# Optimization experiments

Measured on AMD Instinct MI355X. Metric: run time of the kernel, lower is better.

Reference implementation:

```python
import jax, jax.numpy as jnp
import numpy as np

B, N, C = 4, 2048, 1024
H = 16
HD = C // H
SCALE = HD ** -0.5


def setup_inputs() -> dict:
    key = jax.random.key(0)
    k1, k2, k3 = jax.random.split(key, 3)
    x = jax.random.normal(k1, (B, N, C), dtype=jnp.float32)
    qkv_w = jax.random.normal(k2, (3 * C, C), dtype=jnp.float32) * (C ** -0.5)
    proj_w = jax.random.normal(k3, (C, C), dtype=jnp.float32) * (C ** -0.5)
    proj_b = jnp.zeros((C,), dtype=jnp.float32)
    return {"x": x, "qkv_w": qkv_w, "proj_w": proj_w, "proj_b": proj_b}


def reference(x, qkv_w, proj_w, proj_b):
    b, n, c = x.shape
    # qkv: [B, N, 3C] -> [3, B, H, N, HD]
    qkv = jnp.einsum('bnc,dc->bnd', x, qkv_w)
    qkv = qkv.reshape(b, n, 3, H, c // H).transpose(2, 0, 3, 1, 4)
    q, k, v = qkv[0] * SCALE, qkv[1], qkv[2]
    # attention scores [B, H, N, N]
    attn = jnp.einsum('bhqd,bhkd->bhqk', q, k)
    attn = jax.nn.softmax(attn, axis=-1)
    out = jnp.einsum('bhqk,bhkd->bhqd', attn, v)  # [B, H, N, HD]
    out = out.transpose(0, 2, 1, 3).reshape(b, n, c)
    out = jnp.einsum('bnc,dc->bnd', out, proj_w) + proj_b
    return out
```

## Files before the change

kernel.cpp:

```cpp
#include <hip/hip_runtime.h>
#include <math.h>

#define B_  4
#define N_  2048
#define C_  1024
#define H_  16
#define HD_ 64
#define C3_ (3 * C_)
#define QSCALE_ 0.18033688011112042f

typedef float f32x4  __attribute__((ext_vector_type(4)));
typedef float f32x16 __attribute__((ext_vector_type(16)));
typedef short short8 __attribute__((ext_vector_type(8)));
typedef unsigned short ushort8 __attribute__((ext_vector_type(8)));
typedef unsigned int uint2v __attribute__((ext_vector_type(2)));

__device__ inline unsigned short f2bf(float f) {
    union { float f; unsigned u; } v; v.f = f;
    unsigned r = v.u + 0x7fffu + ((v.u >> 16) & 1u);
    return (unsigned short)(r >> 16);
}

__device__ inline unsigned cvtpk_bf16(float lo, float hi) {
    unsigned r;
    asm("v_cvt_pk_bf16_f32 %0, %1, %2" : "=v"(r) : "v"(lo), "v"(hi));
    return r;
}

#define GLD16(gptr, lptr) \
    __builtin_amdgcn_global_load_lds((const __attribute__((address_space(1))) unsigned int*)(gptr), \
                                     (__attribute__((address_space(3))) unsigned int*)(lptr), 16, 0, 0)

__global__ __launch_bounds__(256) void cast_bf16_k(const float* __restrict__ in,
                                                   unsigned short* __restrict__ out,
                                                   int n8, int scale_n8, float scale) {
    int i = blockIdx.x * 256 + threadIdx.x;
    if (i >= n8) return;
    float sc = (i < scale_n8) ? scale : 1.0f;
    const float4* p = (const float4*)in + (size_t)i * 2;
    float4 a = p[0], b = p[1];
    ushort8 o;
    o[0]=f2bf(a.x*sc); o[1]=f2bf(a.y*sc); o[2]=f2bf(a.z*sc); o[3]=f2bf(a.w*sc);
    o[4]=f2bf(b.x*sc); o[5]=f2bf(b.y*sc); o[6]=f2bf(b.z*sc); o[7]=f2bf(b.w*sc);
    *((ushort8*)out + i) = o;
}

__device__ inline void gemm128_core(const unsigned short* __restrict__ A,
                                    const unsigned short* __restrict__ Bm,
                                    int m0, int n0, int K,
                                    char* smem,
                                    f32x4 acc[4][4])
{
    const int tid = threadIdx.x;
    const int lane = tid & 63, w = tid >> 6;
    const int lg = lane >> 4, lr = lane & 15;
    const int wr = (w >> 1) * 64, wc = (w & 1) * 64;
    const int srow = tid >> 2;
    const int scs = (tid & 3) ^ ((srow >> 1) & 3);
    const int lgx = lg ^ ((lr >> 1) & 3);
    const unsigned wbase = (unsigned)(tid & 192) * 16;

    const unsigned short* pa0 = &A[(size_t)(m0 + srow) * K + scs * 8];
    const unsigned short* pa1 = &A[(size_t)(m0 + srow + 64) * K + scs * 8];
    const unsigned short* pb0 = &Bm[(size_t)(n0 + srow) * K + scs * 8];
    const unsigned short* pb1 = &Bm[(size_t)(n0 + srow + 64) * K + scs * 8];

    GLD16(pa0, smem + wbase);
    GLD16(pa1, smem + 4096 + wbase);
    GLD16(pb0, smem + 16384 + wbase);
    GLD16(pb1, smem + 16384 + 4096 + wbase);

    const int NT = K / 32;
    for (int t = 0; t < NT; ++t) {
        __syncthreads();
        const unsigned cur = (unsigned)(t & 1) * 8192;
        if (t + 1 < NT) {
            const unsigned nxt = 8192 - cur;
            const int ko = (t + 1) * 32;
            GLD16(pa0 + ko, smem + nxt + wbase);
            GLD16(pa1 + ko, smem + nxt + 4096 + wbase);
            GLD16(pb0 + ko, smem + 16384 + nxt + wbase);
            GLD16(pb1 + ko, smem + 16384 + nxt + 4096 + wbase);
        }
        const unsigned short* cA = (const unsigned short*)(smem + cur);
        const unsigned short* cB = (const unsigned short*)(smem + 16384 + cur);
        short8 af[4], bf[4];
#pragma unroll
        for (int i = 0; i < 4; ++i) {
            af[i] = *(const short8*)&cA[(wr + i*16 + lr) * 32 + lgx * 8];
            bf[i] = *(const short8*)&cB[(wc + i*16 + lr) * 32 + lgx * 8];
        }
#pragma unroll
        for (int i = 0; i < 4; ++i)
#pragma unroll
            for (int j = 0; j < 4; ++j)
                acc[i][j] = __builtin_amdgcn_mfma_f32_16x16x32_bf16(af[i], bf[j], acc[i][j], 0, 0, 0);
    }
}

__global__ __launch_bounds__(256) void qkv_gemm_k(const unsigned short* __restrict__ x,
                                                  const unsigned short* __restrict__ w,
                                                  unsigned short* __restrict__ outp) {
    __shared__ __align__(16) char smem[32768];
    f32x4 acc[4][4];
    f32x4 z = {0.f, 0.f, 0.f, 0.f};
#pragma unroll
    for (int i = 0; i < 4; ++i)
#pragma unroll
        for (int j = 0; j < 4; ++j) acc[i][j] = z;

    const int m0 = blockIdx.x * 128, n0 = blockIdx.y * 128;
    gemm128_core(x, w, m0, n0, C_, smem, acc);

    const int tid = threadIdx.x, lane = tid & 63, w4 = tid >> 6;
    const int lg = lane >> 4, lr = lane & 15;
    const int wc = (w4 & 1) * 64;
    const int myhalf = w4 >> 1;
    unsigned short* ep = (unsigned short*)smem;

    for (int half = 0; half < 2; ++half) {
        __syncthreads();
        if (myhalf == half) {
#pragma unroll
            for (int mi = 0; mi < 4; ++mi)
#pragma unroll
                for (int ni = 0; ni < 4; ++ni) {
                    const int col = wc + ni * 16 + lr;
                    const int r0 = mi * 16 + lg * 4;
                    unsigned p01 = cvtpk_bf16(acc[mi][ni][0], acc[mi][ni][1]);
                    unsigned p23 = cvtpk_bf16(acc[mi][ni][2], acc[mi][ni][3]);
                    ep[(r0 + 0) * 136 + col] = (unsigned short)p01;
                    ep[(r0 + 1) * 136 + col] = (unsigned short)(p01 >> 16);
                    ep[(r0 + 2) * 136 + col] = (unsigned short)p23;
                    ep[(r0 + 3) * 136 + col] = (unsigned short)(p23 >> 16);
                }
        }
        __syncthreads();
#pragma unroll
        for (int it = 0; it < 4; ++it) {
            int id = it * 256 + tid;
            int rl = id >> 4, ch = id & 15;
            ushort8 o = *(const ushort8*)&ep[rl * 136 + ch * 8];
            *(ushort8*)&outp[(size_t)(m0 + half * 64 + rl) * C3_ + n0 + ch * 8] = o;
        }
    }
}

__global__ __launch_bounds__(256) void vtrans_k(const unsigned short* __restrict__ qkvp,
                                                unsigned short* __restrict__ vt) {
    __shared__ unsigned short st[64 * 72];
    const int tid = threadIdx.x;
    const int n0 = blockIdx.x * 64;
    const int bh = blockIdx.y;
    const int bb = bh >> 4, hh = bh & 15;
    const unsigned short* V = qkvp + (size_t)bb * N_ * C3_ + 2 * C_ + hh * HD_;
    unsigned short* VT = vt + (size_t)bh * HD_ * N_;
    const int r = tid >> 2, c = tid & 3;
    ushort8 v0 = *(const ushort8*)&V[(size_t)(n0 + r) * C3_ + c * 8];
    ushort8 v1 = *(const ushort8*)&V[(size_t)(n0 + r) * C3_ + (c + 4) * 8];
    *(ushort8*)&st[r * 72 + c * 8] = v0;
    *(ushort8*)&st[r * 72 + (c + 4) * 8] = v1;
    __syncthreads();
#pragma unroll
    for (int cc = 0; cc < 2; ++cc) {
        int ch = c + cc * 4;
        ushort8 o;
#pragma unroll
        for (int j = 0; j < 8; ++j) o[j] = st[(ch * 8 + j) * 72 + r];
        *(ushort8*)&VT[(size_t)r * N_ + n0 + ch * 8] = o;
    }
}

__global__ __launch_bounds__(256) void attn_k(const unsigned short* __restrict__ qkvp,
                                              const unsigned short* __restrict__ vt,
                                              unsigned short* __restrict__ aout) {
    __shared__ __align__(16) char smem[32768];

    const int tid = threadIdx.x, lane = tid & 63, w = tid >> 6;
    const int q31 = lane & 31, hi = lane >> 5;
    const int qt = blockIdx.x, h = blockIdx.y, b = blockIdx.z;

    const unsigned short* Qrow = qkvp + (size_t)(b * N_ + qt * 128 + w * 32 + q31) * C3_ + h * HD_;
    const unsigned short* Kbase = qkvp + (size_t)(b * N_) * C3_ + C_ + h * HD_;
    const unsigned short* VT = vt + ((size_t)b * H_ + h) * ((size_t)HD_ * N_);

    short8 qf[4];
#pragma unroll
    for (int ks = 0; ks < 4; ++ks)
        qf[ks] = *(const short8*)&Qrow[ks * 16 + hi * 8];

    f32x16 O0, O1;
#pragma unroll
    for (int r = 0; r < 16; ++r) { O0[r] = 0.f; O1[r] = 0.f; }
    float l_lane = 0.f;

    const int srow = tid >> 3;
    const int scs = (tid & 7) ^ (srow & 7) ^ ((srow >> 3) & 3);
    const unsigned wbase = (unsigned)(tid & 192) * 16;

    const unsigned short* Ksrc = Kbase + (size_t)srow * C3_ + scs * 8;
    const unsigned short* Vsrc = VT + (size_t)srow * N_ + scs * 8;

    const int xq = (q31 & 7) ^ ((q31 >> 3) & 3);
    int fo[4];
#pragma unroll
    for (int ks = 0; ks < 4; ++ks)
        fo[ks] = q31 * 128 + (((2 * ks + hi) ^ xq) * 16);

    GLD16(Ksrc,                          smem + wbase);
    GLD16(Ksrc + (size_t)32 * C3_,       smem + 4096 + wbase);
    GLD16(Vsrc,                          smem + 8192 + wbase);
    GLD16(Vsrc + (size_t)32 * N_,        smem + 12288 + wbase);

    const int NT = N_ / 64;
    for (int t = 0; t < NT; ++t) {
        __syncthreads();
        const unsigned cur = (unsigned)(t & 1) * 16384;
        if (t + 1 < NT) {
            const unsigned nxt = 16384 - cur;
            const size_t k1 = (size_t)(t + 1) * 64;
            GLD16(Ksrc + k1 * C3_,              smem + nxt + wbase);
            GLD16(Ksrc + (k1 + 32) * C3_,       smem + nxt + 4096 + wbase);
            GLD16(Vsrc + k1,                    smem + nxt + 8192 + wbase);
            GLD16(Vsrc + k1 + (size_t)32 * N_,  smem + nxt + 12288 + wbase);
        }
        const char* sK = smem + cur;
        const char* sV = smem + cur + 8192;

        f32x16 S0, S1;
#pragma unroll
        for (int r = 0; r < 16; ++r) { S0[r] = 0.f; S1[r] = 0.f; }
        __builtin_amdgcn_s_setprio(1);
#pragma unroll
        for (int ks = 0; ks < 4; ++ks) {
            short8 kfa = *(const short8*)(sK + fo[ks]);
            short8 kfb = *(const short8*)(sK + 4096 + fo[ks]);
            S0 = __builtin_amdgcn_mfma_f32_32x32x16_bf16(kfa, qf[ks], S0, 0, 0, 0);
            S1 = __builtin_amdgcn_mfma_f32_32x32x16_bf16(kfb, qf[ks], S1, 0, 0, 0);
        }
        __builtin_amdgcn_s_setprio(0);

        float rs = 0.f;
#pragma unroll
        for (int r = 0; r < 16; ++r) {
            float p0 = __builtin_amdgcn_exp2f(S0[r]);
            float p1 = __builtin_amdgcn_exp2f(S1[r]);
            S0[r] = p0; S1[r] = p1;
            rs += p0 + p1;
        }
        l_lane += rs;

        short8 pB[4];
#pragma unroll
        for (int ksk = 0; ksk < 4; ++ksk) {
            const int off = (ksk & 1) * 8;
            float e0, e1, e2, e3, e4, e5, e6, e7;
            if (ksk < 2) { e0=S0[off+0]; e1=S0[off+1]; e2=S0[off+2]; e3=S0[off+3];
                           e4=S0[off+4]; e5=S0[off+5]; e6=S0[off+6]; e7=S0[off+7]; }
            else         { e0=S1[off+0]; e1=S1[off+1]; e2=S1[off+2]; e3=S1[off+3];
                           e4=S1[off+4]; e5=S1[off+5]; e6=S1[off+6]; e7=S1[off+7]; }
            unsigned a_ = cvtpk_bf16(e0, e1);
            unsigned b_ = cvtpk_bf16(e4, e5);
            unsigned c_ = cvtpk_bf16(e2, e3);
            unsigned d_ = cvtpk_bf16(e6, e7);
            uint2v r1 = __builtin_amdgcn_permlane32_swap(a_, b_, false, false);
            uint2v r2 = __builtin_amdgcn_permlane32_swap(c_, d_, false, false);
            union { unsigned u[4]; short8 s; } uu;
            uu.u[0] = r1[0]; uu.u[1] = r2[0]; uu.u[2] = r1[1]; uu.u[3] = r2[1];
            pB[ksk] = uu.s;
        }

        __builtin_amdgcn_s_setprio(1);
#pragma unroll
        for (int ksk = 0; ksk < 4; ++ksk) {
            short8 va0 = *(const short8*)(sV + fo[ksk]);
            short8 va1 = *(const short8*)(sV + 4096 + fo[ksk]);
            O0 = __builtin_amdgcn_mfma_f32_32x32x16_bf16(va0, pB[ksk], O0, 0, 0, 0);
            O1 = __builtin_amdgcn_mfma_f32_32x32x16_bf16(va1, pB[ksk], O1, 0, 0, 0);
        }
        __builtin_amdgcn_s_setprio(0);
    }

    float l = l_lane + __shfl_xor(l_lane, 32);
    __syncthreads();
    unsigned short* epi = (unsigned short*)smem;
    {
        float inv = 1.0f / l;
        const int row = w * 32 + q31;
#pragma unroll
        for (int g = 0; g < 4; ++g) {
            int col0 = 8 * g + 4 * hi;
            *(unsigned*)&epi[row * 72 + col0]          = cvtpk_bf16(O0[4*g+0]*inv, O0[4*g+1]*inv);
            *(unsigned*)&epi[row * 72 + col0 + 2]      = cvtpk_bf16(O0[4*g+2]*inv, O0[4*g+3]*inv);
            *(unsigned*)&epi[row * 72 + 32 + col0]     = cvtpk_bf16(O1[4*g+0]*inv, O1[4*g+1]*inv);
            *(unsigned*)&epi[row * 72 + 32 + col0 + 2] = cvtpk_bf16(O1[4*g+2]*inv, O1[4*g+3]*inv);
        }
    }
    __syncthreads();
#pragma unroll
    for (int it = 0; it < 4; ++it) {
        int id = it * 256 + tid;
        int tk = id >> 3, dc = id & 7;
        ushort8 o = *(const ushort8*)&epi[tk * 72 + dc * 8];
        *(ushort8*)&aout[((size_t)b * N_ + qt * 128 + tk) * C_ + h * HD_ + dc * 8] = o;
    }
}

__global__ __launch_bounds__(256) void proj_gemm_k(const unsigned short* __restrict__ a,
                                                   const unsigned short* __restrict__ w,
                                                   const float* __restrict__ bias,
                                                   float* __restrict__ out) {
    __shared__ __align__(16) char smem[32768];
    f32x4 acc[4][4];
    f32x4 z = {0.f, 0.f, 0.f, 0.f};
#pragma unroll
    for (int i = 0; i < 4; ++i)
#pragma unroll
        for (int j = 0; j < 4; ++j) acc[i][j] = z;

    const int m0 = blockIdx.x * 128, n0 = blockIdx.y * 128;
    gemm128_core(a, w, m0, n0, C_, smem, acc);

    const int lane = threadIdx.x & 63, w4 = threadIdx.x >> 6;
    const int lg = lane >> 4, lr = lane & 15;
    const int wr = (w4 >> 1) * 64, wc = (w4 & 1) * 64;
#pragma unroll
    for (int mi = 0; mi < 4; ++mi)
#pragma unroll
        for (int ni = 0; ni < 4; ++ni) {
            int ch = n0 + wc + ni * 16 + lr;
            float bv = bias[ch];
#pragma unroll
            for (int r = 0; r < 4; ++r) {
                int tok = m0 + wr + mi * 16 + lg * 4 + r;
                out[(size_t)tok * C_ + ch] = acc[mi][ni][r] + bv;
            }
        }
}

extern "C" void kernel_launch(void* const* d_in, const int* in_sizes, int n_in,
                              void* d_out, int out_size, void* d_ws, size_t ws_size,
                              hipStream_t stream) {
    const float* x      = (const float*)d_in[0];
    const float* qkv_w  = (const float*)d_in[1];
    const float* proj_w = (const float*)d_in[2];
    const float* proj_b = (const float*)d_in[3];
    float* out = (float*)d_out;

    unsigned short* x_bf    = (unsigned short*)d_ws;
    unsigned short* wqkv_bf = x_bf + (size_t)B_ * N_ * C_;
    unsigned short* wproj_bf= wqkv_bf + (size_t)3 * C_ * C_;
    unsigned short* qkvp    = wproj_bf + (size_t)C_ * C_;
    unsigned short* vt      = qkvp + (size_t)B_ * N_ * C3_;
    unsigned short* attn    = vt + (size_t)B_ * H_ * HD_ * N_;

    const int nx  = B_ * N_ * C_;
    const int nwq = 3 * C_ * C_;
    const int nwp = C_ * C_;

    cast_bf16_k<<<nx  / 8 / 256, 256, 0, stream>>>(x, x_bf, nx / 8, 0, 1.0f);
    cast_bf16_k<<<nwq / 8 / 256, 256, 0, stream>>>(qkv_w, wqkv_bf, nwq / 8, (C_ * C_) / 8, QSCALE_);
    cast_bf16_k<<<nwp / 8 / 256, 256, 0, stream>>>(proj_w, wproj_bf, nwp / 8, 0, 1.0f);

    qkv_gemm_k<<<dim3((B_ * N_) / 128, C3_ / 128), 256, 0, stream>>>(x_bf, wqkv_bf, qkvp);
    vtrans_k<<<dim3(N_ / 64, B_ * H_), 256, 0, stream>>>(qkvp, vt);
    attn_k<<<dim3(N_ / 128, H_, B_), 256, 0, stream>>>(qkvp, vt, attn);
    proj_gemm_k<<<dim3((B_ * N_) / 128, C_ / 128), 256, 0, stream>>>(attn, wproj_bf, proj_b, out);
}
```

Before: 290.2 us.

## Fuse bf16 casts into one launch and swizzle block order for XCD locality

Merges the three fp32-to-bf16 cast launches into one kernel that picks its source by global index, which removes two launches. The QKV GEMM, attention and projection GEMM now use flattened 1D grids. Block IDs are remapped so that blocks sharing operand tiles (same head/batch, same output column band) land on the same XCD, to improve L2 reuse across MI355X's chiplets. It also seeds the first attention QK MFMA with a zero accumulator instead of zeroing S each iteration. The swizzle assumes 8 XCDs and round-robin dispatch, and the sizes are now hardcoded constants.

```diff
diff --git a/kernel.cpp b/kernel.cpp
--- a/kernel.cpp
+++ b/kernel.cpp
@@ -9,6 +9,11 @@
 #define C3_ (3 * C_)
 #define QSCALE_ 0.18033688011112042f
 
+#define NX8_  1048576
+#define NWQ8_  393216
+#define NWP8_  131072
+#define QS8_   131072
+
 typedef float f32x4  __attribute__((ext_vector_type(4)));
 typedef float f32x16 __attribute__((ext_vector_type(16)));
 typedef short short8 __attribute__((ext_vector_type(8)));
@@ -31,14 +36,24 @@
     __builtin_amdgcn_global_load_lds((const __attribute__((address_space(1))) unsigned int*)(gptr), \
                                      (__attribute__((address_space(3))) unsigned int*)(lptr), 16, 0, 0)
 
-__global__ __launch_bounds__(256) void cast_bf16_k(const float* __restrict__ in,
-                                                   unsigned short* __restrict__ out,
-                                                   int n8, int scale_n8, float scale) {
+__global__ __launch_bounds__(256) void cast_all_k(const float* __restrict__ x,
+                                                  const float* __restrict__ wq,
+                                                  const float* __restrict__ wp,
+                                                  unsigned short* __restrict__ out) {
     int i = blockIdx.x * 256 + threadIdx.x;
-    if (i >= n8) return;
-    float sc = (i < scale_n8) ? scale : 1.0f;
-    const float4* p = (const float4*)in + (size_t)i * 2;
-    float4 a = p[0], b = p[1];
+    const float* src;
+    float sc = 1.0f;
+    if (i < NX8_) {
+        src = x + (size_t)i * 8;
+    } else if (i < NX8_ + NWQ8_) {
+        int j = i - NX8_;
+        src = wq + (size_t)j * 8;
+        if (j < QS8_) sc = QSCALE_;
+    } else {
+        int j = i - NX8_ - NWQ8_;
+        src = wp + (size_t)j * 8;
+    }
+    float4 a = ((const float4*)src)[0], b = ((const float4*)src)[1];
     ushort8 o;
     o[0]=f2bf(a.x*sc); o[1]=f2bf(a.y*sc); o[2]=f2bf(a.z*sc); o[3]=f2bf(a.w*sc);
     o[4]=f2bf(b.x*sc); o[5]=f2bf(b.y*sc); o[6]=f2bf(b.z*sc); o[7]=f2bf(b.w*sc);
@@ -109,7 +124,10 @@
 #pragma unroll
         for (int j = 0; j < 4; ++j) acc[i][j] = z;
 
-    const int m0 = blockIdx.x * 128, n0 = blockIdx.y * 128;
+    const int fid = blockIdx.x;
+    const int xcd = fid & 7, sub = fid >> 3;
+    const int m0 = (xcd * 8 + (sub & 7)) * 128;
+    const int n0 = (sub >> 3) * 128;
     gemm128_core(x, w, m0, n0, C_, smem, acc);
 
     const int tid = threadIdx.x, lane = tid & 63, w4 = tid >> 6;
@@ -178,7 +196,10 @@
 
     const int tid = threadIdx.x, lane = tid & 63, w = tid >> 6;
     const int q31 = lane & 31, hi = lane >> 5;
-    const int qt = blockIdx.x, h = blockIdx.y, b = blockIdx.z;
+
+    const int id = blockIdx.x;
+    const int swz = (id & 7) * 128 + (id >> 3);
+    const int b = swz >> 8, h = (swz >> 4) & 15, qt = swz & 15;
 
     const unsigned short* Qrow = qkvp + (size_t)(b * N_ + qt * 128 + w * 32 + q31) * C3_ + h * HD_;
     const unsigned short* Kbase = qkvp + (size_t)(b * N_) * C3_ + C_ + h * HD_;
@@ -189,9 +210,9 @@
     for (int ks = 0; ks < 4; ++ks)
         qf[ks] = *(const short8*)&Qrow[ks * 16 + hi * 8];
 
-    f32x16 O0, O1;
-#pragma unroll
-    for (int r = 0; r < 16; ++r) { O0[r] = 0.f; O1[r] = 0.f; }
+    f32x16 O0, O1, z16;
+#pragma unroll
+    for (int r = 0; r < 16; ++r) { O0[r] = 0.f; O1[r] = 0.f; z16[r] = 0.f; }
     float l_lane = 0.f;
 
     const int srow = tid >> 3;
@@ -228,11 +249,15 @@
         const char* sV = smem + cur + 8192;
 
         f32x16 S0, S1;
-#pragma unroll
-        for (int r = 0; r < 16; ++r) { S0[r] = 0.f; S1[r] = 0.f; }
         __builtin_amdgcn_s_setprio(1);
-#pragma unroll
-        for (int ks = 0; ks < 4; ++ks) {
+        {
+            short8 kfa = *(const short8*)(sK + fo[0]);
+            short8 kfb = *(const short8*)(sK + 4096 + fo[0]);
+            S0 = __builtin_amdgcn_mfma_f32_32x32x16_bf16(kfa, qf[0], z16, 0, 0, 0);
+            S1 = __builtin_amdgcn_mfma_f32_32x32x16_bf16(kfb, qf[0], z16, 0, 0, 0);
+        }
+#pragma unroll
+        for (int ks = 1; ks < 4; ++ks) {
             short8 kfa = *(const short8*)(sK + fo[ks]);
             short8 kfb = *(const short8*)(sK + 4096 + fo[ks]);
             S0 = __builtin_amdgcn_mfma_f32_32x32x16_bf16(kfa, qf[ks], S0, 0, 0, 0);
@@ -299,8 +324,8 @@
     __syncthreads();
 #pragma unroll
     for (int it = 0; it < 4; ++it) {
-        int id = it * 256 + tid;
-        int tk = id >> 3, dc = id & 7;
+        int id2 = it * 256 + tid;
+        int tk = id2 >> 3, dc = id2 & 7;
         ushort8 o = *(const ushort8*)&epi[tk * 72 + dc * 8];
         *(ushort8*)&aout[((size_t)b * N_ + qt * 128 + tk) * C_ + h * HD_ + dc * 8] = o;
     }
@@ -318,7 +343,10 @@
 #pragma unroll
         for (int j = 0; j < 4; ++j) acc[i][j] = z;
 
-    const int m0 = blockIdx.x * 128, n0 = blockIdx.y * 128;
+    const int fid = blockIdx.x;
+    const int xcd = fid & 7, sub = fid >> 3;
+    const int m0 = (xcd * 8 + (sub & 7)) * 128;
+    const int n0 = (sub >> 3) * 128;
     gemm128_core(a, w, m0, n0, C_, smem, acc);
 
     const int lane = threadIdx.x & 63, w4 = threadIdx.x >> 6;
@@ -354,16 +382,11 @@
     unsigned short* vt      = qkvp + (size_t)B_ * N_ * C3_;
     unsigned short* attn    = vt + (size_t)B_ * H_ * HD_ * N_;
 
-    const int nx  = B_ * N_ * C_;
-    const int nwq = 3 * C_ * C_;
-    const int nwp = C_ * C_;
-
-    cast_bf16_k<<<nx  / 8 / 256, 256, 0, stream>>>(x, x_bf, nx / 8, 0, 1.0f);
-    cast_bf16_k<<<nwq / 8 / 256, 256, 0, stream>>>(qkv_w, wqkv_bf, nwq / 8, (C_ * C_) / 8, QSCALE_);
-    cast_bf16_k<<<nwp / 8 / 256, 256, 0, stream>>>(proj_w, wproj_bf, nwp / 8, 0, 1.0f);
-
-    qkv_gemm_k<<<dim3((B_ * N_) / 128, C3_ / 128), 256, 0, stream>>>(x_bf, wqkv_bf, qkvp);
+    const int ncast = NX8_ + NWQ8_ + NWP8_;
+    cast_all_k<<<ncast / 256, 256, 0, stream>>>(x, qkv_w, proj_w, x_bf);
+
+    qkv_gemm_k<<<1536, 256, 0, stream>>>(x_bf, wqkv_bf, qkvp);
     vtrans_k<<<dim3(N_ / 64, B_ * H_), 256, 0, stream>>>(qkvp, vt);
-    attn_k<<<dim3(N_ / 128, H_, B_), 256, 0, stream>>>(qkvp, vt, attn);
-    proj_gemm_k<<<dim3((B_ * N_) / 128, C_ / 128), 256, 0, stream>>>(attn, wproj_bf, proj_b, out);
-}
+    attn_k<<<1024, 256, 0, stream>>>(qkvp, vt, attn);
+    proj_gemm_k<<<512, 256, 0, stream>>>(attn, wproj_bf, proj_b, out);
+}
```

New measurement: 294.0 us. About the same (+1.3%).
